# Kernel optimization log

Measured on AMD Instinct MI355X. Metric: run time of the kernel, lower is better.

## Reference

```python
import jax, jax.numpy as jnp
import numpy as np

N_NODES = 100000


def gcn_conv(x, W, b, src, dst, norm, n):
    # x: [N, Fin] -> [N, Fout]; PyG GCNConv: linear, then normalized scatter-add
    h = x @ W                                   # [N, Fout]
    msgs = h[src] * norm[:, None]               # gather + degree-normalize, [E2, Fout]
    out = jax.ops.segment_sum(msgs, dst, num_segments=n)  # scatter-add
    return out + b


def _norm_and_loops(edge_index, n):
    # add self-loops and compute symmetric normalization deg^-1/2 * deg^-1/2
    src = jnp.concatenate([edge_index[0], jnp.arange(n)])
    dst = jnp.concatenate([edge_index[1], jnp.arange(n)])
    deg = jax.ops.segment_sum(jnp.ones_like(dst, dtype=jnp.float32), dst, num_segments=n)
    dinv = jnp.where(deg > 0, jax.lax.rsqrt(jnp.maximum(deg, 1.0)), 0.0)
    norm = dinv[src] * dinv[dst]
    return src, dst, norm


def setup_inputs() -> dict:
    key = jax.random.key(0)
    ks = jax.random.split(key, 10)
    F_IN, H, C = 128, 128, 40
    x = jax.random.normal(ks[0], (N_NODES, F_IN), dtype=jnp.float32)
    edge_index = jax.random.randint(ks[1], (2, 3200000), 0, N_NODES, dtype=jnp.int64)
    def glorot(k, fan_in, fan_out):
        s = jnp.sqrt(6.0 / (fan_in + fan_out))
        return jax.random.uniform(k, (fan_in, fan_out), jnp.float32, -s, s)
    return {
        'x': x,
        'edge_index': edge_index,
        'W1': glorot(ks[2], F_IN, H), 'b1': jnp.zeros((H,), jnp.float32),
        'W2': glorot(ks[3], H, H),    'b2': jnp.zeros((H,), jnp.float32),
        'W3': glorot(ks[4], H, H),    'b3': jnp.zeros((H,), jnp.float32),
        'Wc': glorot(ks[5], H, C),    'bc': jnp.zeros((C,), jnp.float32),
    }


def reference(x, edge_index, W1, b1, W2, b2, W3, b3, Wc, bc):
    n = x.shape[0]
    src, dst, norm = _norm_and_loops(edge_index, n)
    h = jnp.tanh(gcn_conv(x, W1, b1, src, dst, norm, n))
    h = jnp.tanh(gcn_conv(h, W2, b2, src, dst, norm, n))
    h = jnp.tanh(gcn_conv(h, W3, b3, src, dst, norm, n))
    out = h @ Wc + bc
    return (out, h)
```

## Files before the change

### kernel.cpp

```cpp
#include <hip/hip_runtime.h>
#include <hip/hip_fp16.h>
#include <math.h>

#define H 128
#define BSTRIDE 5120
#define NPH 25

typedef _Float16 f16x8 __attribute__((ext_vector_type(8)));
typedef float f32x4 __attribute__((ext_vector_type(4)));


__global__ __launch_bounds__(256) void bin_kernel(const int* __restrict__ src,
        const int* __restrict__ dst, int* __restrict__ bucketFill,
        int* __restrict__ packed, int E, int nbk) {
    __shared__ int hcnt[1024];
    __shared__ int base[1024];
    __shared__ int cur[1024];
    int tid = threadIdx.x;
    for (int i = tid; i < nbk; i += 256) { hcnt[i] = 0; cur[i] = 0; }
    __syncthreads();
    int e0 = blockIdx.x * 8192;
    int e1 = min(e0 + 8192, E);
    for (int e = e0 + tid; e < e1; e += 256)
        atomicAdd(&hcnt[dst[e] >> 7], 1);
    __syncthreads();
    for (int i = tid; i < nbk; i += 256) {
        int c = hcnt[i];
        base[i] = c ? atomicAdd(&bucketFill[i], c) : 0;
    }
    __syncthreads();
    for (int e = e0 + tid; e < e1; e += 256) {
        int d = dst[e], s = src[e];
        int b = d >> 7;
        int r = atomicAdd(&cur[b], 1);
        packed[b * BSTRIDE + base[b] + r] = ((d & 127) << 17) | s;
    }
}

__global__ __launch_bounds__(256) void fine_kernel(const int* __restrict__ packed,
        const int* __restrict__ bucketFill,
        int* __restrict__ rowptr, int* __restrict__ col, float* __restrict__ dinv,
        int N, int E) {
    __shared__ int cnt[128 * NPH];
    __shared__ int cur[128 * NPH];
    __shared__ int lcnt[128], lofs[128];
    __shared__ int red[256];
    int b = blockIdx.x;
    int tid = threadIdx.x;
    int m = bucketFill[b]; if (m > BSTRIDE) m = BSTRIDE;
    int n0 = b << 7;

    int psum = 0;
    for (int i = tid; i < b; i += 256) psum += bucketFill[i];
    red[tid] = psum;
    for (int i = tid; i < 128 * NPH; i += 256) cnt[i] = 0;
    __syncthreads();
    #pragma unroll
    for (int off = 128; off > 0; off >>= 1) {
        if (tid < off) red[tid] += red[tid + off];
        __syncthreads();
    }
    int base = red[0];
    if (b == 0 && tid == 0) rowptr[N] = E;

    const int* pk = packed + (size_t)b * BSTRIDE;
    for (int i = tid; i < m; i += 256) {
        int p = pk[i];
        int ld = p >> 17, s = p & 131071;
        atomicAdd(&cnt[ld * NPH + (s >> 12)], 1);
    }
    __syncthreads();
    if (tid < 128) {
        int t = 0;
        #pragma unroll
        for (int q = 0; q < NPH; ++q) t += cnt[tid * NPH + q];
        lcnt[tid] = t;
    }
    __syncthreads();
    if (tid == 0) {
        int acc = 0;
        #pragma unroll 4
        for (int i = 0; i < 128; ++i) { lofs[i] = acc; acc += lcnt[i]; }
    }
    __syncthreads();
    if (tid < 128) {
        int o = lofs[tid];
        #pragma unroll
        for (int q = 0; q < NPH; ++q) {
            int c = cnt[tid * NPH + q];
            cur[tid * NPH + q] = o;
            o += c;
        }
        int node = n0 + tid;
        if (node < N) {
            rowptr[node] = base + lofs[tid];
            dinv[node] = rsqrtf((float)(lcnt[tid] + 1));
        }
    }
    __syncthreads();
    for (int i = tid; i < m; i += 256) {
        int p = pk[i];
        int ld = p >> 17, s = p & 131071;
        int r = atomicAdd(&cur[ld * NPH + (s >> 12)], 1);
        col[base + r] = s;
    }
}


__global__ __launch_bounds__(256) void gemm128_kernel(const float* __restrict__ A,
        const float* __restrict__ W, const float* __restrict__ scale,
        unsigned short* __restrict__ C, int N) {
    __shared__ _Float16 Ah[64][H + 8];
    __shared__ _Float16 Wt[H][H + 8];
    int tid = threadIdx.x;
    int r0 = blockIdx.x * 64;

    #pragma unroll
    for (int i = 0; i < 8; ++i) {
        int lin = tid + i * 256;
        int r = lin >> 5;
        int c4 = (lin & 31) << 2;
        float4 v = make_float4(0.f, 0.f, 0.f, 0.f);
        if (r0 + r < N) v = *(const float4*)&A[(size_t)(r0 + r) * H + c4];
        _Float16* ap = &Ah[r][c4];
        ap[0] = (_Float16)v.x; ap[1] = (_Float16)v.y;
        ap[2] = (_Float16)v.z; ap[3] = (_Float16)v.w;
    }
    #pragma unroll
    for (int i = 0; i < 64; ++i) {
        int lin = i * 256 + tid;
        int k = lin >> 7, n = lin & 127;
        Wt[n][k] = (_Float16)W[lin];
    }
    __syncthreads();

    int wid = tid >> 6;
    int lane = tid & 63;
    int cb = wid << 5;
    int m16 = lane & 15;
    int kg = lane >> 4;

    f32x4 acc[4][2];
    #pragma unroll
    for (int rt = 0; rt < 4; ++rt)
        #pragma unroll
        for (int ct = 0; ct < 2; ++ct)
            acc[rt][ct] = (f32x4){0.f, 0.f, 0.f, 0.f};

    #pragma unroll
    for (int kc = 0; kc < 4; ++kc) {
        int kbase = kc * 32 + kg * 8;
        f16x8 afr[4], bfr[2];
        #pragma unroll
        for (int rt = 0; rt < 4; ++rt)
            afr[rt] = *(const f16x8*)&Ah[rt * 16 + m16][kbase];
        #pragma unroll
        for (int ct = 0; ct < 2; ++ct)
            bfr[ct] = *(const f16x8*)&Wt[cb + ct * 16 + m16][kbase];
        #pragma unroll
        for (int rt = 0; rt < 4; ++rt)
            #pragma unroll
            for (int ct = 0; ct < 2; ++ct)
                acc[rt][ct] = __builtin_amdgcn_mfma_f32_16x16x32_f16(
                        afr[rt], bfr[ct], acc[rt][ct], 0, 0, 0);
    }

    #pragma unroll
    for (int rt = 0; rt < 4; ++rt) {
        int rowb = r0 + rt * 16 + (lane >> 4) * 4;
        #pragma unroll
        for (int reg = 0; reg < 4; ++reg) {
            int grow = rowb + reg;
            if (grow < N) {
                float s = scale[grow];
                unsigned short* Crow = C + (size_t)grow * H + cb + (lane & 15);
                __half h0 = __float2half_rn(acc[rt][0][reg] * s);
                __half h1 = __float2half_rn(acc[rt][1][reg] * s);
                Crow[0]  = *(unsigned short*)&h0;
                Crow[16] = *(unsigned short*)&h1;
            }
        }
    }
}


__device__ inline void add8(float* a, uint4 v) {
    float2 f;
    f = __half22float2(*(const __half2*)&v.x); a[0] += f.x; a[1] += f.y;
    f = __half22float2(*(const __half2*)&v.y); a[2] += f.x; a[3] += f.y;
    f = __half22float2(*(const __half2*)&v.z); a[4] += f.x; a[5] += f.y;
    f = __half22float2(*(const __half2*)&v.w); a[6] += f.x; a[7] += f.y;
}

__global__ __launch_bounds__(256) void spmm_kernel(const unsigned short* __restrict__ lin,
        const int* __restrict__ rowptr, const int* __restrict__ col,
        const float* __restrict__ dinv, const float* __restrict__ bias,
        float* __restrict__ out, int N) {
    int tid = threadIdx.x;
    int node = blockIdx.x * 16 + (tid >> 4);
    if (node >= N) return;
    int cq = tid & 15;

    int beg = rowptr[node];
    int end = rowptr[node + 1];

    const uint4* linv = (const uint4*)lin;

    float acc[8];
    {
        uint4 sv = linv[(size_t)node * 16 + cq];
        float2 f;
        f = __half22float2(*(const __half2*)&sv.x); acc[0] = f.x; acc[1] = f.y;
        f = __half22float2(*(const __half2*)&sv.y); acc[2] = f.x; acc[3] = f.y;
        f = __half22float2(*(const __half2*)&sv.z); acc[4] = f.x; acc[5] = f.y;
        f = __half22float2(*(const __half2*)&sv.w); acc[6] = f.x; acc[7] = f.y;
    }

    int e = beg;
    for (; e + 4 <= end; e += 4) {
        int s0 = col[e], s1 = col[e + 1], s2 = col[e + 2], s3 = col[e + 3];
        uint4 v0 = linv[(size_t)s0 * 16 + cq];
        uint4 v1 = linv[(size_t)s1 * 16 + cq];
        uint4 v2 = linv[(size_t)s2 * 16 + cq];
        uint4 v3 = linv[(size_t)s3 * 16 + cq];
        add8(acc, v0);
        add8(acc, v1);
        add8(acc, v2);
        add8(acc, v3);
    }
    for (; e < end; ++e) {
        uint4 v = linv[(size_t)col[e] * 16 + cq];
        add8(acc, v);
    }

    float d = dinv[node];
    int c8 = cq << 3;
    float4 r0, r1;
    r0.x = tanhf(fmaf(acc[0], d, bias[c8 + 0]));
    r0.y = tanhf(fmaf(acc[1], d, bias[c8 + 1]));
    r0.z = tanhf(fmaf(acc[2], d, bias[c8 + 2]));
    r0.w = tanhf(fmaf(acc[3], d, bias[c8 + 3]));
    r1.x = tanhf(fmaf(acc[4], d, bias[c8 + 4]));
    r1.y = tanhf(fmaf(acc[5], d, bias[c8 + 5]));
    r1.z = tanhf(fmaf(acc[6], d, bias[c8 + 6]));
    r1.w = tanhf(fmaf(acc[7], d, bias[c8 + 7]));
    float4* op = (float4*)out + (size_t)node * 32 + (cq << 1);
    op[0] = r0;
    op[1] = r1;
}


__global__ __launch_bounds__(256) void classifier_kernel(const float* __restrict__ h,
        const float* __restrict__ Wc, const float* __restrict__ bc,
        float* __restrict__ out, int N, int Cout) {
    __shared__ float As[64][H + 1];
    int tid = threadIdx.x;
    int r0 = blockIdx.x * 64;

    #pragma unroll
    for (int i = 0; i < 8; ++i) {
        int lin = tid + i * 256;
        int r = lin >> 5;
        int c4 = (lin & 31) << 2;
        float4 v = make_float4(0.f, 0.f, 0.f, 0.f);
        if (r0 + r < N) v = *(const float4*)&h[(size_t)(r0 + r) * H + c4];
        As[r][c4 + 0] = v.x; As[r][c4 + 1] = v.y;
        As[r][c4 + 2] = v.z; As[r][c4 + 3] = v.w;
    }
    __syncthreads();

    int row = tid & 63;
    int c0 = __builtin_amdgcn_readfirstlane((tid >> 6) * 10);

    float acc[10];
    #pragma unroll
    for (int j = 0; j < 10; ++j) acc[j] = bc[c0 + j];

    for (int k = 0; k < H; ++k) {
        float a = As[row][k];
        #pragma unroll
        for (int j = 0; j < 10; ++j)
            acc[j] = fmaf(a, Wc[k * Cout + c0 + j], acc[j]);
    }

    int gr = r0 + row;
    if (gr < N) {
        float* orow = out + (size_t)gr * Cout + c0;
        #pragma unroll
        for (int j = 0; j < 10; ++j) orow[j] = acc[j];
    }
}


extern "C" void kernel_launch(void* const* d_in, const int* in_sizes, int n_in,
                              void* d_out, int out_size, void* d_ws, size_t ws_size,
                              hipStream_t stream) {
    const float* x  = (const float*)d_in[0];
    const int* eidx = (const int*)d_in[1];
    const float* W1 = (const float*)d_in[2];
    const float* b1 = (const float*)d_in[3];
    const float* W2 = (const float*)d_in[4];
    const float* b2 = (const float*)d_in[5];
    const float* W3 = (const float*)d_in[6];
    const float* b3 = (const float*)d_in[7];
    const float* Wc = (const float*)d_in[8];
    const float* bc = (const float*)d_in[9];

    int N    = in_sizes[0] / H;
    int E    = in_sizes[1] / 2;
    int Cout = in_sizes[8] / H;
    int nbk  = (N + 127) >> 7;

    const int* srcp = eidx;
    const int* dstp = eidx + E;

    float* out  = (float*)d_out;
    float* hOut = out + (size_t)N * Cout;

    char* p = (char*)d_ws;
    float* hAf      = (float*)p;  p += (size_t)N * H * 4;
    int*   col      = (int*)p;    p += (size_t)E * 4;
    int*   rowptr   = (int*)p;    p += (size_t)(N + 1) * 4;
    float* dinv     = (float*)p;  p += (size_t)N * 4;
    int*   bFill    = (int*)p;    p += 1024 * 4;
    unsigned short* hA = (unsigned short*)hAf;
    int*   packed   = (int*)hAf;

    int gg = (N + 63) / 64;
    int gs = (N + 15) / 16;
    int gb = (E + 8191) / 8192;

    hipMemsetAsync(bFill, 0, (size_t)nbk * 4, stream);
    bin_kernel<<<gb, 256, 0, stream>>>(srcp, dstp, bFill, packed, E, nbk);
    fine_kernel<<<nbk, 256, 0, stream>>>(packed, bFill, rowptr, col, dinv, N, E);

    gemm128_kernel<<<gg, 256, 0, stream>>>(x, W1, dinv, hA, N);
    spmm_kernel<<<gs, 256, 0, stream>>>(hA, rowptr, col, dinv, b1, hOut, N);
    gemm128_kernel<<<gg, 256, 0, stream>>>(hOut, W2, dinv, hA, N);
    spmm_kernel<<<gs, 256, 0, stream>>>(hA, rowptr, col, dinv, b2, hOut, N);
    gemm128_kernel<<<gg, 256, 0, stream>>>(hOut, W3, dinv, hA, N);
    spmm_kernel<<<gs, 256, 0, stream>>>(hA, rowptr, col, dinv, b3, hOut, N);
    classifier_kernel<<<gg, 256, 0, stream>>>(hOut, Wc, bc, out, N, Cout);
}
```

Before: 705.3 us.

## Store intermediate activations in fp16 and fuse classifier into final SpMM

New measurement: 677.7 us. -3.9%, faster.

```diff
diff --git a/kernel.cpp b/kernel.cpp
--- a/kernel.cpp
+++ b/kernel.cpp
@@ -3,6 +3,7 @@
 #include <math.h>
 
 #define H 128
+#define COUT 40
 #define BSTRIDE 5120
 #define NPH 25
 
@@ -107,6 +108,62 @@
 }
 
 
+__device__ inline unsigned pack2(float x, float y) {
+    __half2 h = __floats2half2_rn(x, y);
+    return *(unsigned*)&h;
+}
+
+__device__ inline void gemm_core_and_store(_Float16 (*Ah)[H + 8], _Float16 (*Wt)[H + 8],
+        const float* scale, unsigned short* C, int r0, int tid, int N) {
+    int wid = tid >> 6;
+    int lane = tid & 63;
+    int cb = wid << 5;
+    int m16 = lane & 15;
+    int kg = lane >> 4;
+
+    f32x4 acc[4][2];
+    #pragma unroll
+    for (int rt = 0; rt < 4; ++rt)
+        #pragma unroll
+        for (int ct = 0; ct < 2; ++ct)
+            acc[rt][ct] = (f32x4){0.f, 0.f, 0.f, 0.f};
+
+    #pragma unroll
+    for (int kc = 0; kc < 4; ++kc) {
+        int kbase = kc * 32 + kg * 8;
+        f16x8 afr[4], bfr[2];
+        #pragma unroll
+        for (int rt = 0; rt < 4; ++rt)
+            afr[rt] = *(const f16x8*)&Ah[rt * 16 + m16][kbase];
+        #pragma unroll
+        for (int ct = 0; ct < 2; ++ct)
+            bfr[ct] = *(const f16x8*)&Wt[cb + ct * 16 + m16][kbase];
+        #pragma unroll
+        for (int rt = 0; rt < 4; ++rt)
+            #pragma unroll
+            for (int ct = 0; ct < 2; ++ct)
+                acc[rt][ct] = __builtin_amdgcn_mfma_f32_16x16x32_f16(
+                        afr[rt], bfr[ct], acc[rt][ct], 0, 0, 0);
+    }
+
+    #pragma unroll
+    for (int rt = 0; rt < 4; ++rt) {
+        int rowb = r0 + rt * 16 + kg * 4;
+        #pragma unroll
+        for (int reg = 0; reg < 4; ++reg) {
+            int grow = rowb + reg;
+            if (grow < N) {
+                float s = scale[grow];
+                unsigned short* Crow = C + (size_t)grow * H + cb + m16;
+                __half h0 = __float2half_rn(acc[rt][0][reg] * s);
+                __half h1 = __float2half_rn(acc[rt][1][reg] * s);
+                Crow[0]  = *(unsigned short*)&h0;
+                Crow[16] = *(unsigned short*)&h1;
+            }
+        }
+    }
+}
+
 __global__ __launch_bounds__(256) void gemm128_kernel(const float* __restrict__ A,
         const float* __restrict__ W, const float* __restrict__ scale,
         unsigned short* __restrict__ C, int N) {
@@ -133,54 +190,34 @@
         Wt[n][k] = (_Float16)W[lin];
     }
     __syncthreads();
-
-    int wid = tid >> 6;
-    int lane = tid & 63;
-    int cb = wid << 5;
-    int m16 = lane & 15;
-    int kg = lane >> 4;
-
-    f32x4 acc[4][2];
-    #pragma unroll
-    for (int rt = 0; rt < 4; ++rt)
-        #pragma unroll
-        for (int ct = 0; ct < 2; ++ct)
-            acc[rt][ct] = (f32x4){0.f, 0.f, 0.f, 0.f};
-
-    #pragma unroll
-    for (int kc = 0; kc < 4; ++kc) {
-        int kbase = kc * 32 + kg * 8;
-        f16x8 afr[4], bfr[2];
-        #pragma unroll
-        for (int rt = 0; rt < 4; ++rt)
-            afr[rt] = *(const f16x8*)&Ah[rt * 16 + m16][kbase];
-        #pragma unroll
-        for (int ct = 0; ct < 2; ++ct)
-            bfr[ct] = *(const f16x8*)&Wt[cb + ct * 16 + m16][kbase];
-        #pragma unroll
-        for (int rt = 0; rt < 4; ++rt)
-            #pragma unroll
-            for (int ct = 0; ct < 2; ++ct)
-                acc[rt][ct] = __builtin_amdgcn_mfma_f32_16x16x32_f16(
-                        afr[rt], bfr[ct], acc[rt][ct], 0, 0, 0);
-    }
-
-    #pragma unroll
-    for (int rt = 0; rt < 4; ++rt) {
-        int rowb = r0 + rt * 16 + (lane >> 4) * 4;
-        #pragma unroll
-        for (int reg = 0; reg < 4; ++reg) {
-            int grow = rowb + reg;
-            if (grow < N) {
-                float s = scale[grow];
-                unsigned short* Crow = C + (size_t)grow * H + cb + (lane & 15);
-                __half h0 = __float2half_rn(acc[rt][0][reg] * s);
-                __half h1 = __float2half_rn(acc[rt][1][reg] * s);
-                Crow[0]  = *(unsigned short*)&h0;
-                Crow[16] = *(unsigned short*)&h1;
-            }
-        }
-    }
+    gemm_core_and_store(Ah, Wt, scale, C, r0, tid, N);
+}
+
+__global__ __launch_bounds__(256) void gemm128f16_kernel(const unsigned short* __restrict__ A,
+        const float* __restrict__ W, const float* __restrict__ scale,
+        unsigned short* __restrict__ C, int N) {
+    __shared__ _Float16 Ah[64][H + 8];
+    __shared__ _Float16 Wt[H][H + 8];
+    int tid = threadIdx.x;
+    int r0 = blockIdx.x * 64;
+
+    #pragma unroll
+    for (int i = 0; i < 4; ++i) {
+        int lin = tid + i * 256;
+        int r = lin >> 4;
+        int c8 = (lin & 15) << 3;
+        uint4 v = make_uint4(0, 0, 0, 0);
+        if (r0 + r < N) v = *(const uint4*)&A[(size_t)(r0 + r) * H + c8];
+        *(uint4*)&Ah[r][c8] = v;
+    }
+    #pragma unroll
+    for (int i = 0; i < 64; ++i) {
+        int lin = i * 256 + tid;
+        int k = lin >> 7, n = lin & 127;
+        Wt[n][k] = (_Float16)W[lin];
+    }
+    __syncthreads();
+    gemm_core_and_store(Ah, Wt, scale, C, r0, tid, N);
 }
 
 
@@ -192,21 +229,10 @@
     f = __half22float2(*(const __half2*)&v.w); a[6] += f.x; a[7] += f.y;
 }
 
-__global__ __launch_bounds__(256) void spmm_kernel(const unsigned short* __restrict__ lin,
-        const int* __restrict__ rowptr, const int* __restrict__ col,
-        const float* __restrict__ dinv, const float* __restrict__ bias,
-        float* __restrict__ out, int N) {
-    int tid = threadIdx.x;
-    int node = blockIdx.x * 16 + (tid >> 4);
-    if (node >= N) return;
-    int cq = tid & 15;
-
+__device__ inline void spmm_gather(const uint4* linv, const int* rowptr,
+        const int* col, int node, int cq, float* acc) {
     int beg = rowptr[node];
     int end = rowptr[node + 1];
-
-    const uint4* linv = (const uint4*)lin;
-
-    float acc[8];
     {
         uint4 sv = linv[(size_t)node * 16 + cq];
         float2 f;
@@ -215,7 +241,6 @@
         f = __half22float2(*(const __half2*)&sv.z); acc[4] = f.x; acc[5] = f.y;
         f = __half22float2(*(const __half2*)&sv.w); acc[6] = f.x; acc[7] = f.y;
     }
-
     int e = beg;
     for (; e + 4 <= end; e += 4) {
         int s0 = col[e], s1 = col[e + 1], s2 = col[e + 2], s3 = col[e + 3];
@@ -232,62 +257,89 @@
         uint4 v = linv[(size_t)col[e] * 16 + cq];
         add8(acc, v);
     }
+}
+
+__global__ __launch_bounds__(256) void spmm_h16_kernel(const unsigned short* __restrict__ lin,
+        const int* __restrict__ rowptr, const int* __restrict__ col,
+        const float* __restrict__ dinv, const float* __restrict__ bias,
+        unsigned short* __restrict__ h16, int N) {
+    int tid = threadIdx.x;
+    int node = blockIdx.x * 16 + (tid >> 4);
+    if (node >= N) return;
+    int cq = tid & 15;
+
+    float acc[8];
+    spmm_gather((const uint4*)lin, rowptr, col, node, cq, acc);
 
     float d = dinv[node];
     int c8 = cq << 3;
-    float4 r0, r1;
-    r0.x = tanhf(fmaf(acc[0], d, bias[c8 + 0]));
-    r0.y = tanhf(fmaf(acc[1], d, bias[c8 + 1]));
-    r0.z = tanhf(fmaf(acc[2], d, bias[c8 + 2]));
-    r0.w = tanhf(fmaf(acc[3], d, bias[c8 + 3]));
-    r1.x = tanhf(fmaf(acc[4], d, bias[c8 + 4]));
-    r1.y = tanhf(fmaf(acc[5], d, bias[c8 + 5]));
-    r1.z = tanhf(fmaf(acc[6], d, bias[c8 + 6]));
-    r1.w = tanhf(fmaf(acc[7], d, bias[c8 + 7]));
-    float4* op = (float4*)out + (size_t)node * 32 + (cq << 1);
-    op[0] = r0;
-    op[1] = r1;
-}
-
-
-__global__ __launch_bounds__(256) void classifier_kernel(const float* __restrict__ h,
+    float t0 = tanhf(fmaf(acc[0], d, bias[c8 + 0]));
+    float t1 = tanhf(fmaf(acc[1], d, bias[c8 + 1]));
+    float t2 = tanhf(fmaf(acc[2], d, bias[c8 + 2]));
+    float t3 = tanhf(fmaf(acc[3], d, bias[c8 + 3]));
+    float t4 = tanhf(fmaf(acc[4], d, bias[c8 + 4]));
+    float t5 = tanhf(fmaf(acc[5], d, bias[c8 + 5]));
+    float t6 = tanhf(fmaf(acc[6], d, bias[c8 + 6]));
+    float t7 = tanhf(fmaf(acc[7], d, bias[c8 + 7]));
+    uint4 w;
+    w.x = pack2(t0, t1);
+    w.y = pack2(t2, t3);
+    w.z = pack2(t4, t5);
+    w.w = pack2(t6, t7);
+    ((uint4*)h16)[(size_t)node * 16 + cq] = w;
+}
+
+__global__ __launch_bounds__(256) void spmm_fused_kernel(const unsigned short* __restrict__ lin,
+        const int* __restrict__ rowptr, const int* __restrict__ col,
+        const float* __restrict__ dinv, const float* __restrict__ bias,
         const float* __restrict__ Wc, const float* __restrict__ bc,
-        float* __restrict__ out, int N, int Cout) {
-    __shared__ float As[64][H + 1];
-    int tid = threadIdx.x;
-    int r0 = blockIdx.x * 64;
-
-    #pragma unroll
-    for (int i = 0; i < 8; ++i) {
-        int lin = tid + i * 256;
-        int r = lin >> 5;
-        int c4 = (lin & 31) << 2;
-        float4 v = make_float4(0.f, 0.f, 0.f, 0.f);
-        if (r0 + r < N) v = *(const float4*)&h[(size_t)(r0 + r) * H + c4];
-        As[r][c4 + 0] = v.x; As[r][c4 + 1] = v.y;
-        As[r][c4 + 2] = v.z; As[r][c4 + 3] = v.w;
-    }
-    __syncthreads();
-
-    int row = tid & 63;
-    int c0 = __builtin_amdgcn_readfirstlane((tid >> 6) * 10);
-
-    float acc[10];
-    #pragma unroll
-    for (int j = 0; j < 10; ++j) acc[j] = bc[c0 + j];
-
+        float* __restrict__ hout, float* __restrict__ out, int N) {
+    __shared__ float Hs[16][132];
+    __shared__ float WcS[H * COUT];
+    int tid = threadIdx.x;
+    int node = blockIdx.x * 16 + (tid >> 4);
+    int cq = tid & 15;
+    bool act = node < N;
+
+    for (int i = tid; i < H * COUT; i += 256) WcS[i] = Wc[i];
+
+    float acc[8];
+    if (act) spmm_gather((const uint4*)lin, rowptr, col, node, cq, acc);
+
+    int nl = tid >> 4;
+    int c8 = cq << 3;
+    if (act) {
+        float d = dinv[node];
+        float4 r0, r1;
+        r0.x = tanhf(fmaf(acc[0], d, bias[c8 + 0]));
+        r0.y = tanhf(fmaf(acc[1], d, bias[c8 + 1]));
+        r0.z = tanhf(fmaf(acc[2], d, bias[c8 + 2]));
+        r0.w = tanhf(fmaf(acc[3], d, bias[c8 + 3]));
+        r1.x = tanhf(fmaf(acc[4], d, bias[c8 + 4]));
+        r1.y = tanhf(fmaf(acc[5], d, bias[c8 + 5]));
+        r1.z = tanhf(fmaf(acc[6], d, bias[c8 + 6]));
+        r1.w = tanhf(fmaf(acc[7], d, bias[c8 + 7]));
+        float4* op = (float4*)hout + (size_t)node * 32 + (cq << 1);
+        op[0] = r0;
+        op[1] = r1;
+        *(float4*)&Hs[nl][c8]     = r0;
+        *(float4*)&Hs[nl][c8 + 4] = r1;
+    }
+    __syncthreads();
+
+    float s0 = 0.f, s1 = 0.f, s2 = 0.f;
     for (int k = 0; k < H; ++k) {
-        float a = As[row][k];
-        #pragma unroll
-        for (int j = 0; j < 10; ++j)
-            acc[j] = fmaf(a, Wc[k * Cout + c0 + j], acc[j]);
-    }
-
-    int gr = r0 + row;
-    if (gr < N) {
-        float* orow = out + (size_t)gr * Cout + c0;
-        #pragma unroll
-        for (int j = 0; j < 10; ++j) orow[j] = acc[j];
+        float h = Hs[nl][k];
+        const float* wr = &WcS[k * COUT];
+        s0 = fmaf(h, wr[cq], s0);
+        s1 = fmaf(h, wr[cq + 16], s1);
+        if (cq < 8) s2 = fmaf(h, wr[cq + 32], s2);
+    }
+    if (act) {
+        float* orow = out + (size_t)node * COUT;
+        orow[cq]      = s0 + bc[cq];
+        orow[cq + 16] = s1 + bc[cq + 16];
+        if (cq < 8) orow[cq + 32] = s2 + bc[cq + 32];
     }
 }
 
@@ -308,14 +360,14 @@
 
     int N    = in_sizes[0] / H;
     int E    = in_sizes[1] / 2;
-    int Cout = in_sizes[8] / H;
     int nbk  = (N + 127) >> 7;
 
     const int* srcp = eidx;
     const int* dstp = eidx + E;
 
     float* out  = (float*)d_out;
-    float* hOut = out + (size_t)N * Cout;
+    float* hOut = out + (size_t)N * COUT;
+    unsigned short* h16 = (unsigned short*)hOut;
 
     char* p = (char*)d_ws;
     float* hAf      = (float*)p;  p += (size_t)N * H * 4;
@@ -335,10 +387,9 @@
     fine_kernel<<<nbk, 256, 0, stream>>>(packed, bFill, rowptr, col, dinv, N, E);
 
     gemm128_kernel<<<gg, 256, 0, stream>>>(x, W1, dinv, hA, N);
-    spmm_kernel<<<gs, 256, 0, stream>>>(hA, rowptr, col, dinv, b1, hOut, N);
-    gemm128_kernel<<<gg, 256, 0, stream>>>(hOut, W2, dinv, hA, N);
-    spmm_kernel<<<gs, 256, 0, stream>>>(hA, rowptr, col, dinv, b2, hOut, N);
-    gemm128_kernel<<<gg, 256, 0, stream>>>(hOut, W3, dinv, hA, N);
-    spmm_kernel<<<gs, 256, 0, stream>>>(hA, rowptr, col, dinv, b3, hOut, N);
-    classifier_kernel<<<gg, 256, 0, stream>>>(hOut, Wc, bc, out, N, Cout);
-}
+    spmm_h16_kernel<<<gs, 256, 0, stream>>>(hA, rowptr, col, dinv, b1, h16, N);
+    gemm128f16_kernel<<<gg, 256, 0, stream>>>(h16, W2, dinv, hA, N);
+    spmm_h16_kernel<<<gs, 256, 0, stream>>>(hA, rowptr, col, dinv, b2, h16, N);
+    gemm128f16_kernel<<<gg, 256, 0, stream>>>(h16, W3, dinv, hA, N);
+    spmm_fused_kernel<<<gs, 256, 0, stream>>>(hA, rowptr, col, dinv, b3, Wc, bc, hOut, out, N);
+}
```
